# Optimization experiments

Hardware: AMD Instinct MI355X
Metric: run time of the kernel (lower is better)

## Reference

```python
import jax, jax.numpy as jnp
import numpy as np

NEG = jnp.float32(-1e30)  # finite stand-in for -inf (grad-safe)
BLANK = 0


def setup_inputs() -> dict:
    key = jax.random.key(0)
    k1, k2, k3, k4 = jax.random.split(key, 4)
    B, T, V, S = 64, 1024, 128, 256
    logits = jax.random.normal(k1, (B, T, V), dtype=jnp.float32)
    log_probs = jax.nn.log_softmax(logits, axis=-1)  # valid log-probs like a model head
    log_probs_length = jax.random.randint(k2, (B,), 768, T + 1)
    text_encoded = jax.random.randint(k3, (B, S), 1, V)  # labels exclude blank=0
    text_encoded_length = jax.random.randint(k4, (B,), 64, S + 1)
    return {
        "log_probs": log_probs,
        "log_probs_length": log_probs_length,
        "text_encoded": text_encoded,
        "text_encoded_length": text_encoded_length,
    }


def _ctc_loss(log_probs, input_lengths, targets, target_lengths):
    """CTC loss, matching torch.nn.CTCLoss(blank=0, reduction='mean', zero_infinity=True)."""
    B, T, V = log_probs.shape
    S = targets.shape[1]
    L2 = 2 * S + 1  # extended label sequence: blank-interleaved

    # extended labels ext[b, s]: blank at even s, target[(s-1)//2] at odd s
    ext = jnp.full((B, L2), BLANK, dtype=targets.dtype)
    ext = ext.at[:, 1::2].set(targets)

    # gather per-step log-prob of each extended label: [B, T, L2]
    lp_ext = jnp.take_along_axis(
        log_probs, jnp.broadcast_to(ext[:, None, :], (B, T, L2)), axis=2
    )

    pos = jnp.arange(L2)
    valid_s = pos[None, :] < (2 * target_lengths[:, None] + 1)  # [B, L2]
    ext_m2 = jnp.pad(ext, ((0, 0), (2, 0)), constant_values=BLANK)[:, :-2]
    # skip transition s-2 -> s allowed only at non-blank (odd) positions with differing labels
    skip_mask = (pos[None, :] >= 2) & (pos[None, :] % 2 == 1) & (ext != ext_m2)

    alpha0 = jnp.full((B, L2), NEG, dtype=log_probs.dtype)
    alpha0 = alpha0.at[:, 0].set(lp_ext[:, 0, 0])
    alpha0 = alpha0.at[:, 1].set(jnp.where(target_lengths > 0, lp_ext[:, 0, 1], NEG))
    alpha0 = jnp.where(valid_s, alpha0, NEG)

    lp_ext_T = jnp.moveaxis(lp_ext, 1, 0)  # [T, B, L2]

    def step(alpha, x):
        lp_t, t = x
        s1 = jnp.pad(alpha, ((0, 0), (1, 0)), constant_values=NEG)[:, :-1]
        s2 = jnp.pad(alpha, ((0, 0), (2, 0)), constant_values=NEG)[:, :-2]
        a = jnp.logaddexp(alpha, s1)
        a = jnp.where(skip_mask, jnp.logaddexp(a, s2), a)
        new = jnp.where(valid_s, a + lp_t, NEG)
        # freeze alpha for samples whose input sequence has ended
        new = jnp.where((t < input_lengths)[:, None], new, alpha)
        return new, None

    alpha, _ = jax.lax.scan(step, alpha0, (lp_ext_T[1:], jnp.arange(1, T)))

    L = target_lengths
    idx1 = (2 * L)[:, None]
    idx0 = jnp.maximum(2 * L - 1, 0)[:, None]
    a_blank = jnp.take_along_axis(alpha, idx1, axis=1)[:, 0]
    a_label = jnp.take_along_axis(alpha, idx0, axis=1)[:, 0]
    ll = jnp.logaddexp(a_blank, jnp.where(L > 0, a_label, NEG))
    loss_b = -ll
    # zero_infinity: zero out infeasible alignments
    loss_b = jnp.where(loss_b > 1e29, jnp.float32(0.0), loss_b)
    # reduction='mean': divide each loss by its target length, then batch-mean
    return jnp.mean(loss_b / jnp.maximum(L, 1).astype(log_probs.dtype))


def reference(log_probs, log_probs_length, text_encoded, text_encoded_length):
    return _ctc_loss(log_probs, log_probs_length, text_encoded, text_encoded_length)
```

## Files before the change

### kernel.cpp

```cpp
#include <hip/hip_runtime.h>

constexpr int B_ = 64;
constexpr int T_ = 1024;
constexpr int V_ = 128;
constexpr int S_ = 256;
constexpr int GRING = 64;
constexpr int NTAG = 16;
constexpr int ROWF = 384;
constexpr int NGW = 3;
constexpr float INV_LN2 = 1.4426950408889634f;
constexpr float LN2 = 0.6931471805599453f;

#define WS_DUMPF(W, b) ((W) + 64 + (size_t)(b) * 640)
#define WS_DUMPB(W, b) ((W) + 64 + 64 * 640 + (size_t)(b) * 640)
#define WS_KARR(W)     ((int*)((W) + 64 + 2 * 64 * 640))

#define WG_SCOPE __HIP_MEMORY_SCOPE_WORKGROUP

__device__ __forceinline__ void poll_eq(int* p, int want) {
    while (__hip_atomic_load(p, __ATOMIC_RELAXED, WG_SCOPE) != want)
        __builtin_amdgcn_s_sleep(1);
}

template <int CTRL>
__device__ __forceinline__ float dpp_mov0(float x) {
    return __int_as_float(__builtin_amdgcn_update_dpp(
        0, __float_as_int(x), CTRL, 0xF, 0xF, false));
}
template <int CTRL>
__device__ __forceinline__ float dpp_max(float x) {
    const float s = __int_as_float(__builtin_amdgcn_update_dpp(
        __float_as_int(x), __float_as_int(x), CTRL, 0xF, 0xF, false));
    return fmaxf(x, s);
}

__device__ __forceinline__ int wave_rescale(float a[10], int& K) {
    float mx = a[0];
    #pragma unroll
    for (int k = 1; k < 10; ++k) mx = fmaxf(mx, a[k]);
    mx = dpp_max<0x111>(mx);
    mx = dpp_max<0x112>(mx);
    mx = dpp_max<0x114>(mx);
    mx = dpp_max<0x118>(mx);
    mx = dpp_max<0x142>(mx);
    mx = dpp_max<0x143>(mx);
    const float mall = __int_as_float(
        __builtin_amdgcn_readlane(__float_as_int(mx), 63));
    int e;
    (void)frexpf(mall, &e);
    const int ks = (mall > 0.0f) ? (124 - e) : 0;
    #pragma unroll
    for (int k = 0; k < 10; ++k) a[k] = ldexpf(a[k], ks);
    K += ks;
    return ks;
}

__global__ __launch_bounds__(256) void ctc_scan(
    const float* __restrict__ lp,
    const int* __restrict__ in_len,
    const int* __restrict__ tgt,
    const int* __restrict__ tgt_len,
    float* __restrict__ W)
{
    const int b    = blockIdx.x & 63;
    const int dir  = blockIdx.x >> 6;
    const int tid  = threadIdx.x;
    const int wid  = tid >> 6;
    const int lane = tid & 63;

    __shared__ float ring[GRING * ROWF];
    __shared__ int   tags[NTAG];
    __shared__ int   cons;

    const int L  = tgt_len[b];
    const int Tb = in_len[b];
    const float* lpb = lp + (size_t)b * T_ * V_;
    const int* tg = tgt + b * S_;

    const int tm = (Tb - 2) >> 1;
    const int Uf = tm;
    const int Ub = Tb - 2 - tm;
    const int U  = dir ? Ub : Uf;

    if (tid == 0) cons = 0;
    if (tid < NTAG) tags[tid] = -1;
    __syncthreads();

    if (wid >= 1) {
        const int q = wid - 1;

        int   perm[5], oddc[5];
        float vmask[5];
        #pragma unroll
        for (int c = 0; c < 5; ++c) {
            const int j = 5 * lane + c;
            if (j < L) { const int lb = tg[j]; perm[c] = lb >> 1; oddc[c] = lb & 1; vmask[c] = 1.0f; }
            else       { perm[c] = 0; oddc[c] = 0; vmask[c] = 0.0f; }
        }

        float2 R0[4], R1[4];
        auto issue = [&](float2 (&Rb)[4], int m) {
            const int n = min(4, U - 4 * m);
            #pragma unroll
            for (int r = 0; r < 4; ++r) {
                if (r < n) {
                    const int u = 4 * m + 1 + r;
                    const int t = dir ? (Tb - 1 - u) : u;
                    Rb[r] = *(const float2*)(lpb + (size_t)t * V_ + 2 * lane);
                }
            }
        };
        auto process = [&](float2 (&Rb)[4], int m) {
            while (__hip_atomic_load(&cons, __ATOMIC_RELAXED, WG_SCOPE) < 4 * m - 60)
                __builtin_amdgcn_s_sleep(1);
            const int n = min(4, U - 4 * m);
            #pragma unroll
            for (int r = 0; r < 4; ++r) {
                if (r < n) {
                    const float e0 = __builtin_exp2f(Rb[r].x * INV_LN2);
                    const float e1 = __builtin_exp2f(Rb[r].y * INV_LN2);
                    const float p0 = __int_as_float(
                        __builtin_amdgcn_readfirstlane(__float_as_int(e0)));
                    float gv[5];
                    #pragma unroll
                    for (int c = 0; c < 5; ++c) {
                        const float lo = __shfl(e0, perm[c], 64);
                        const float hi = __shfl(e1, perm[c], 64);
                        gv[c] = vmask[c] * (oddc[c] ? hi : lo);
                    }
                    float* rb = ring + ((4 * m + r) & (GRING - 1)) * ROWF;
                    ((float2*)rb)[lane]         = make_float2(p0,    gv[0]);
                    ((float2*)(rb + 128))[lane] = make_float2(gv[1], gv[2]);
                    ((float2*)(rb + 256))[lane] = make_float2(gv[3], gv[4]);
                }
            }
            asm volatile("s_waitcnt lgkmcnt(0)" ::: "memory");
            if (lane == 0)
                __hip_atomic_store(&tags[m & (NTAG - 1)], m, __ATOMIC_RELAXED, WG_SCOPE);
        };

        int m = q;
        if (4 * m + 1 <= U) {
            issue(R0, m);
            if (4 * (m + NGW) + 1 <= U) issue(R1, m + NGW);
            while (true) {
                process(R0, m);
                if (4 * (m + 2 * NGW) + 1 <= U) issue(R0, m + 2 * NGW);
                m += NGW;
                if (4 * m + 1 > U) break;
                process(R1, m);
                if (4 * (m + 2 * NGW) + 1 <= U) issue(R1, m + 2 * NGW);
                m += NGW;
                if (4 * m + 1 > U) break;
            }
        }
        return;
    }

    float2 S[4][12];
    auto readBlock = [&](int set, int m) {
        const int base = ((4 * m) & (GRING - 1)) * ROWF + 2 * lane;
        #pragma unroll
        for (int r = 0; r < 4; ++r)
            #pragma unroll
            for (int pl = 0; pl < 3; ++pl)
                S[set][r * 3 + pl] =
                    *(const float2*)&ring[base + r * ROWF + pl * 128];
    };

    if (dir == 0) {
        float skipf[5];
        #pragma unroll
        for (int c = 0; c < 5; ++c) {
            const int j = 5 * lane + c;
            skipf[c] = (j >= 1 && j < L && tg[j] != tg[j - 1]) ? 1.0f : 0.0f;
        }
        float a[10];
        #pragma unroll
        for (int k = 0; k < 10; ++k) a[k] = 0.0f;
        {
            const float p00 = __builtin_exp2f(lpb[0] * INV_LN2);
            const float p01 = __builtin_exp2f(lpb[tg[0]] * INV_LN2);
            if (lane == 0) { a[0] = p00; a[1] = p01; }
        }
        float u9n = 0.0f;
        int K = 0;

        auto rowCore = [&](float2 c0, float2 c1, float2 c2) {
            const float u9 = u9n;
            const float p0 = c0.x;
            a[9] = (a[9] + a[8] + skipf[4] * a[7]) * c2.y;
            u9n = dpp_mov0<0x138>(a[9]);
            a[8] = (a[8] + a[7]) * p0;
            a[7] = (a[7] + a[6] + skipf[3] * a[5]) * c2.x;
            a[6] = (a[6] + a[5]) * p0;
            a[5] = (a[5] + a[4] + skipf[2] * a[3]) * c1.y;
            a[4] = (a[4] + a[3]) * p0;
            a[3] = (a[3] + a[2] + skipf[1] * a[1]) * c1.x;
            a[2] = (a[2] + a[1]) * p0;
            a[1] = (a[1] + a[0] + skipf[0] * u9) * c0.y;
            a[0] = (a[0] + u9) * p0;
        };
        auto row4 = [&](int set) {
            #pragma unroll
            for (int r = 0; r < 4; ++r)
                rowCore(S[set][r * 3], S[set][r * 3 + 1], S[set][r * 3 + 2]);
        };
        auto body = [&](int m, int setc, int setp) {
            if (4 * (m + 3) + 1 <= Uf) {
                poll_eq(&tags[(m + 3) & (NTAG - 1)], m + 3);
                readBlock(setp, m + 3);
            }
            row4(setc);
            if (lane == 0)
                __hip_atomic_store(&cons, 4 * m + 4, __ATOMIC_RELAXED, WG_SCOPE);
        };

        const int MB4 = (Uf / 4) & ~3;
        poll_eq(&tags[0], 0); readBlock(0, 0);
        poll_eq(&tags[1], 1); readBlock(1, 1);
        poll_eq(&tags[2], 2); readBlock(2, 2);
        for (int mb = 0; mb < MB4; mb += 4) {
            body(mb + 0, 0, 3);
            body(mb + 1, 1, 0);
            { const int ks = wave_rescale(a, K); u9n = ldexpf(u9n, ks); }
            body(mb + 2, 2, 1);
            body(mb + 3, 3, 2);
            { const int ks = wave_rescale(a, K); u9n = ldexpf(u9n, ks); }
        }
        #pragma unroll
        for (int r = 0; r < 4; ++r)
            if (4 * MB4 + 1 + r <= Uf)
                rowCore(S[0][r * 3], S[0][r * 3 + 1], S[0][r * 3 + 2]);
        #pragma unroll
        for (int r = 0; r < 4; ++r)
            if (4 * MB4 + 5 + r <= Uf)
                rowCore(S[1][r * 3], S[1][r * 3 + 1], S[1][r * 3 + 2]);
        { const int ks = wave_rescale(a, K); u9n = ldexpf(u9n, ks); }
        #pragma unroll
        for (int r = 0; r < 4; ++r)
            if (4 * MB4 + 9 + r <= Uf)
                rowCore(S[2][r * 3], S[2][r * 3 + 1], S[2][r * 3 + 2]);
        for (int u = 4 * MB4 + 13; u <= Uf; ++u) {
            const int bu = (u - 1) >> 2;
            poll_eq(&tags[bu & (NTAG - 1)], bu);
            const int base = ((u - 1) & (GRING - 1)) * ROWF + 2 * lane;
            const float2 c0 = *(const float2*)&ring[base];
            const float2 c1 = *(const float2*)&ring[base + 128];
            const float2 c2 = *(const float2*)&ring[base + 256];
            rowCore(c0, c1, c2);
        }

        float* dump = WS_DUMPF(W, b);
        #pragma unroll
        for (int k = 0; k < 10; ++k) dump[10 * lane + k] = a[k];
        if (lane == 0) WS_KARR(W)[b] = K;
    } else {
        float sB[5];
        #pragma unroll
        for (int c = 0; c < 5; ++c) {
            const int j = 5 * lane + c + 1;
            sB[c] = (j < L && tg[j] != tg[j - 1]) ? 1.0f : 0.0f;
        }
        float g[10];
        #pragma unroll
        for (int k = 0; k < 10; ++k) g[k] = 0.0f;
        {
            const float pb = __builtin_exp2f(lpb[(size_t)(Tb - 1) * V_] * INV_LN2);
            const float pl = __builtin_exp2f(lpb[(size_t)(Tb - 1) * V_ + tg[L - 1]] * INV_LN2);
            #pragma unroll
            for (int k = 0; k < 10; ++k) {
                const int s = 10 * lane + k;
                if (s == 2 * L)     g[k] = pb;
                if (s == 2 * L - 1) g[k] = pl;
            }
        }
        float d0n = dpp_mov0<0x130>(g[0]);
        float d1n = dpp_mov0<0x130>(g[1]);
        int K = 0;

        auto rowCore = [&](float2 c0, float2 c1, float2 c2) {
            const float d0 = d0n, d1 = d1n;
            const float p0 = c0.x;
            g[0] = (g[0] + g[1]) * p0;
            g[1] = (g[1] + g[2] + sB[0] * g[3]) * c0.y;
            d0n = dpp_mov0<0x130>(g[0]);
            d1n = dpp_mov0<0x130>(g[1]);
            g[2] = (g[2] + g[3]) * p0;
            g[3] = (g[3] + g[4] + sB[1] * g[5]) * c1.x;
            g[4] = (g[4] + g[5]) * p0;
            g[5] = (g[5] + g[6] + sB[2] * g[7]) * c1.y;
            g[6] = (g[6] + g[7]) * p0;
            g[7] = (g[7] + g[8] + sB[3] * g[9]) * c2.x;
            g[8] = (g[8] + g[9]) * p0;
            g[9] = (g[9] + d0 + sB[4] * d1) * c2.y;
        };
        auto row4 = [&](int set) {
            #pragma unroll
            for (int r = 0; r < 4; ++r)
                rowCore(S[set][r * 3], S[set][r * 3 + 1], S[set][r * 3 + 2]);
        };
        auto body = [&](int m, int setc, int setp) {
            if (4 * (m + 3) + 1 <= Ub) {
                poll_eq(&tags[(m + 3) & (NTAG - 1)], m + 3);
                readBlock(setp, m + 3);
            }
            row4(setc);
            if (lane == 0)
                __hip_atomic_store(&cons, 4 * m + 4, __ATOMIC_RELAXED, WG_SCOPE);
        };

        const int MB4 = (Ub / 4) & ~3;
        poll_eq(&tags[0], 0); readBlock(0, 0);
        poll_eq(&tags[1], 1); readBlock(1, 1);
        poll_eq(&tags[2], 2); readBlock(2, 2);
        for (int mb = 0; mb < MB4; mb += 4) {
            body(mb + 0, 0, 3);
            body(mb + 1, 1, 0);
            { const int ks = wave_rescale(g, K);
              d0n = ldexpf(d0n, ks); d1n = ldexpf(d1n, ks); }
            body(mb + 2, 2, 1);
            body(mb + 3, 3, 2);
            { const int ks = wave_rescale(g, K);
              d0n = ldexpf(d0n, ks); d1n = ldexpf(d1n, ks); }
        }
        #pragma unroll
        for (int r = 0; r < 4; ++r)
            if (4 * MB4 + 1 + r <= Ub)
                rowCore(S[0][r * 3], S[0][r * 3 + 1], S[0][r * 3 + 2]);
        #pragma unroll
        for (int r = 0; r < 4; ++r)
            if (4 * MB4 + 5 + r <= Ub)
                rowCore(S[1][r * 3], S[1][r * 3 + 1], S[1][r * 3 + 2]);
        { const int ks = wave_rescale(g, K);
          d0n = ldexpf(d0n, ks); d1n = ldexpf(d1n, ks); }
        #pragma unroll
        for (int r = 0; r < 4; ++r)
            if (4 * MB4 + 9 + r <= Ub)
                rowCore(S[2][r * 3], S[2][r * 3 + 1], S[2][r * 3 + 2]);
        for (int u = 4 * MB4 + 13; u <= Ub; ++u) {
            const int bu = (u - 1) >> 2;
            poll_eq(&tags[bu & (NTAG - 1)], bu);
            const int base = ((u - 1) & (GRING - 1)) * ROWF + 2 * lane;
            const float2 c0 = *(const float2*)&ring[base];
            const float2 c1 = *(const float2*)&ring[base + 128];
            const float2 c2 = *(const float2*)&ring[base + 256];
            rowCore(c0, c1, c2);
        }

        {
            const float d0 = d0n, d1 = d1n;
            g[0] = g[0] + g[1];
            g[1] = g[1] + g[2] + sB[0] * g[3];
            g[2] = g[2] + g[3];
            g[3] = g[3] + g[4] + sB[1] * g[5];
            g[4] = g[4] + g[5];
            g[5] = g[5] + g[6] + sB[2] * g[7];
            g[6] = g[6] + g[7];
            g[7] = g[7] + g[8] + sB[3] * g[9];
            g[8] = g[8] + g[9];
            g[9] = g[9] + d0 + sB[4] * d1;
        }
        float* dump = WS_DUMPB(W, b);
        #pragma unroll
        for (int k = 0; k < 10; ++k) dump[10 * lane + k] = g[k];
        if (lane == 0) WS_KARR(W)[64 + b] = K;
    }
}

__global__ void ctc_join_kernel(const float* __restrict__ W_const,
                                const int* __restrict__ tgt_len,
                                float* __restrict__ lossArr) {
    const int b = blockIdx.x;
    const int lane = threadIdx.x;
    float* W = const_cast<float*>(W_const);
    const float* dA = WS_DUMPF(W, b);
    const float* dB = WS_DUMPB(W, b);
    double sum = 0.0;
    #pragma unroll
    for (int k = 0; k < 10; ++k)
        sum += (double)dA[10 * lane + k] * (double)dB[10 * lane + k];
    #pragma unroll
    for (int d = 1; d < 64; d <<= 1) sum += __shfl_xor(sum, d, 64);
    if (lane == 0) {
        const int L = tgt_len[b];
        const int KF = WS_KARR(W)[b];
        const int KB = WS_KARR(W)[64 + b];
        float loss = 0.0f;
        if (sum > 0.0) {
            const long long ub = __double_as_longlong(sum);
            const int ex = (int)((ub >> 52) & 2047) - 1023;
            const double f = __longlong_as_double(
                (ub & 0x000FFFFFFFFFFFFFLL) | 0x3FF0000000000000LL);
            const float ll2 = __builtin_log2f((float)f)
                            + (float)(ex - KF - KB);
            loss = -(ll2 * LN2);
            if (!(loss <= 1e29f)) loss = 0.0f;
        }
        lossArr[b] = loss / (float)L;
    }
}

__global__ void ctc_reduce_kernel(const float* __restrict__ ws, float* __restrict__ out) {
    float v = ws[threadIdx.x];
    #pragma unroll
    for (int o = 32; o > 0; o >>= 1) v += __shfl_down(v, o);
    if (threadIdx.x == 0) out[0] = v / (float)B_;
}

extern "C" void kernel_launch(void* const* d_in, const int* in_sizes, int n_in,
                              void* d_out, int out_size, void* d_ws, size_t ws_size,
                              hipStream_t stream) {
    const float* lp      = (const float*)d_in[0];
    const int*   in_len  = (const int*)d_in[1];
    const int*   tgt     = (const int*)d_in[2];
    const int*   tgt_len = (const int*)d_in[3];
    float* W   = (float*)d_ws;
    float* out = (float*)d_out;

    ctc_scan<<<2 * B_, 256, 0, stream>>>(lp, in_len, tgt, tgt_len, W);
    ctc_join_kernel<<<B_, 64, 0, stream>>>(W, tgt_len, W);
    ctc_reduce_kernel<<<1, 64, 0, stream>>>(W, out);
}
```

Measured before the change: 130.2 us.

## Move label gather from producer waves into consumer LDS reads, shrink ring rows

Producer waves now only exponentiate each time-step row and store the raw 128-entry probability row into LDS. The label permutation moves to the consumer wave, which gathers by label offset straight from the ring. This shrinks ring rows from 384 to 128 floats and drops the per-row shuffle work in the producers. The block goes from four waves to three, and consumer prefetch depth falls from three blocks to one. The consumer's critical serial path now carries the indexed LDS gathers and extra vmask multiplies, and the shallower prefetch may expose latency.

```diff
diff --git a/kernel.cpp b/kernel.cpp
--- a/kernel.cpp
+++ b/kernel.cpp
@@ -6,8 +6,8 @@
 constexpr int S_ = 256;
 constexpr int GRING = 64;
 constexpr int NTAG = 16;
-constexpr int ROWF = 384;
-constexpr int NGW = 3;
+constexpr int RW = 128;
+constexpr int NGW = 2;
 constexpr float INV_LN2 = 1.4426950408889634f;
 constexpr float LN2 = 0.6931471805599453f;
 
@@ -55,7 +55,7 @@
     return ks;
 }
 
-__global__ __launch_bounds__(256) void ctc_scan(
+__global__ __launch_bounds__(192) void ctc_scan(
     const float* __restrict__ lp,
     const int* __restrict__ in_len,
     const int* __restrict__ tgt,
@@ -68,7 +68,7 @@
     const int wid  = tid >> 6;
     const int lane = tid & 63;
 
-    __shared__ float ring[GRING * ROWF];
+    __shared__ float ring[GRING * RW];
     __shared__ int   tags[NTAG];
     __shared__ int   cons;
 
@@ -88,15 +88,6 @@
 
     if (wid >= 1) {
         const int q = wid - 1;
-
-        int   perm[5], oddc[5];
-        float vmask[5];
-        #pragma unroll
-        for (int c = 0; c < 5; ++c) {
-            const int j = 5 * lane + c;
-            if (j < L) { const int lb = tg[j]; perm[c] = lb >> 1; oddc[c] = lb & 1; vmask[c] = 1.0f; }
-            else       { perm[c] = 0; oddc[c] = 0; vmask[c] = 0.0f; }
-        }
 
         float2 R0[4], R1[4];
         auto issue = [&](float2 (&Rb)[4], int m) {
@@ -119,19 +110,8 @@
                 if (r < n) {
                     const float e0 = __builtin_exp2f(Rb[r].x * INV_LN2);
                     const float e1 = __builtin_exp2f(Rb[r].y * INV_LN2);
-                    const float p0 = __int_as_float(
-                        __builtin_amdgcn_readfirstlane(__float_as_int(e0)));
-                    float gv[5];
-                    #pragma unroll
-                    for (int c = 0; c < 5; ++c) {
-                        const float lo = __shfl(e0, perm[c], 64);
-                        const float hi = __shfl(e1, perm[c], 64);
-                        gv[c] = vmask[c] * (oddc[c] ? hi : lo);
-                    }
-                    float* rb = ring + ((4 * m + r) & (GRING - 1)) * ROWF;
-                    ((float2*)rb)[lane]         = make_float2(p0,    gv[0]);
-                    ((float2*)(rb + 128))[lane] = make_float2(gv[1], gv[2]);
-                    ((float2*)(rb + 256))[lane] = make_float2(gv[3], gv[4]);
+                    float* rb = ring + ((4 * m + r) & (GRING - 1)) * RW;
+                    ((float2*)rb)[lane] = make_float2(e0, e1);
                 }
             }
             asm volatile("s_waitcnt lgkmcnt(0)" ::: "memory");
@@ -157,15 +137,31 @@
         return;
     }
 
-    float2 S[4][12];
+    int   off[5];
+    float vmask[5];
+    #pragma unroll
+    for (int c = 0; c < 5; ++c) {
+        const int j = 5 * lane + c;
+        if (j < L) { off[c] = tg[j]; vmask[c] = 1.0f; }
+        else       { off[c] = 0;     vmask[c] = 0.0f; }
+    }
+
+    float S2[2][24];
     auto readBlock = [&](int set, int m) {
-        const int base = ((4 * m) & (GRING - 1)) * ROWF + 2 * lane;
-        #pragma unroll
-        for (int r = 0; r < 4; ++r)
-            #pragma unroll
-            for (int pl = 0; pl < 3; ++pl)
-                S[set][r * 3 + pl] =
-                    *(const float2*)&ring[base + r * ROWF + pl * 128];
+        const int base = ((4 * m) & (GRING - 1)) * RW;
+        #pragma unroll
+        for (int r = 0; r < 4; ++r) {
+            S2[set][r * 6 + 0] = ring[base + r * RW];
+            #pragma unroll
+            for (int c = 0; c < 5; ++c)
+                S2[set][r * 6 + 1 + c] = ring[base + r * RW + off[c]];
+        }
+    };
+    auto readRowDirect = [&](int u, float (&v)[6]) {
+        const int base = ((u - 1) & (GRING - 1)) * RW;
+        v[0] = ring[base];
+        #pragma unroll
+        for (int c = 0; c < 5; ++c) v[1 + c] = ring[base + off[c]];
     };
 
     if (dir == 0) {
@@ -204,57 +200,51 @@
         auto row4 = [&](int set) {
             #pragma unroll
             for (int r = 0; r < 4; ++r)
-                rowCore(S[set][r * 3], S[set][r * 3 + 1], S[set][r * 3 + 2]);
+                rowCore(make_float2(S2[set][r*6+0], vmask[0]*S2[set][r*6+1]),
+                        make_float2(vmask[1]*S2[set][r*6+2], vmask[2]*S2[set][r*6+3]),
+                        make_float2(vmask[3]*S2[set][r*6+4], vmask[4]*S2[set][r*6+5]));
         };
         auto body = [&](int m, int setc, int setp) {
-            if (4 * (m + 3) + 1 <= Uf) {
-                poll_eq(&tags[(m + 3) & (NTAG - 1)], m + 3);
-                readBlock(setp, m + 3);
+            if (4 * (m + 1) + 1 <= Uf) {
+                poll_eq(&tags[(m + 1) & (NTAG - 1)], m + 1);
+                readBlock(setp, m + 1);
             }
             row4(setc);
             if (lane == 0)
                 __hip_atomic_store(&cons, 4 * m + 4, __ATOMIC_RELAXED, WG_SCOPE);
         };
 
-        const int MB4 = (Uf / 4) & ~3;
+        const int MB2 = (Uf / 4) & ~1;
         poll_eq(&tags[0], 0); readBlock(0, 0);
-        poll_eq(&tags[1], 1); readBlock(1, 1);
-        poll_eq(&tags[2], 2); readBlock(2, 2);
-        for (int mb = 0; mb < MB4; mb += 4) {
-            body(mb + 0, 0, 3);
+        for (int mb = 0; mb < MB2; mb += 2) {
+            body(mb + 0, 0, 1);
             body(mb + 1, 1, 0);
             { const int ks = wave_rescale(a, K); u9n = ldexpf(u9n, ks); }
-            body(mb + 2, 2, 1);
-            body(mb + 3, 3, 2);
-            { const int ks = wave_rescale(a, K); u9n = ldexpf(u9n, ks); }
         }
         #pragma unroll
         for (int r = 0; r < 4; ++r)
-            if (4 * MB4 + 1 + r <= Uf)
-                rowCore(S[0][r * 3], S[0][r * 3 + 1], S[0][r * 3 + 2]);
-        #pragma unroll
-        for (int r = 0; r < 4; ++r)
-            if (4 * MB4 + 5 + r <= Uf)
-                rowCore(S[1][r * 3], S[1][r * 3 + 1], S[1][r * 3 + 2]);
-        { const int ks = wave_rescale(a, K); u9n = ldexpf(u9n, ks); }
-        #pragma unroll
-        for (int r = 0; r < 4; ++r)
-            if (4 * MB4 + 9 + r <= Uf)
-                rowCore(S[2][r * 3], S[2][r * 3 + 1], S[2][r * 3 + 2]);
-        for (int u = 4 * MB4 + 13; u <= Uf; ++u) {
+            if (4 * MB2 + 1 + r <= Uf)
+                rowCore(make_float2(S2[0][r*6+0], vmask[0]*S2[0][r*6+1]),
+                        make_float2(vmask[1]*S2[0][r*6+2], vmask[2]*S2[0][r*6+3]),
+                        make_float2(vmask[3]*S2[0][r*6+4], vmask[4]*S2[0][r*6+5]));
+        for (int u = 4 * (MB2 + 1) + 1; u <= Uf; ++u) {
             const int bu = (u - 1) >> 2;
             poll_eq(&tags[bu & (NTAG - 1)], bu);
-            const int base = ((u - 1) & (GRING - 1)) * ROWF + 2 * lane;
-            const float2 c0 = *(const float2*)&ring[base];
-            const float2 c1 = *(const float2*)&ring[base + 128];
-            const float2 c2 = *(const float2*)&ring[base + 256];
-            rowCore(c0, c1, c2);
-        }
+            float v[6];
+            readRowDirect(u, v);
+            rowCore(make_float2(v[0], vmask[0]*v[1]),
+                    make_float2(vmask[1]*v[2], vmask[2]*v[3]),
+                    make_float2(vmask[3]*v[4], vmask[4]*v[5]));
+        }
+        { const int ks = wave_rescale(a, K); u9n = ldexpf(u9n, ks); }
 
         float* dump = WS_DUMPF(W, b);
         #pragma unroll
         for (int k = 0; k < 10; ++k) dump[10 * lane + k] = a[k];
-        if (lane == 0) WS_KARR(W)[b] = K;
+        if (lane == 0) {
+            WS_KARR(W)[b] = K;
+            __hip_atomic_store(&cons, Uf + 64, __ATOMIC_RELAXED, WG_SCOPE);
+        }
     } else {
         float sB[5];
         #pragma unroll
@@ -298,55 +288,45 @@
         auto row4 = [&](int set) {
             #pragma unroll
             for (int r = 0; r < 4; ++r)
-                rowCore(S[set][r * 3], S[set][r * 3 + 1], S[set][r * 3 + 2]);
+                rowCore(make_float2(S2[set][r*6+0], vmask[0]*S2[set][r*6+1]),
+                        make_float2(vmask[1]*S2[set][r*6+2], vmask[2]*S2[set][r*6+3]),
+                        make_float2(vmask[3]*S2[set][r*6+4], vmask[4]*S2[set][r*6+5]));
         };
         auto body = [&](int m, int setc, int setp) {
-            if (4 * (m + 3) + 1 <= Ub) {
-                poll_eq(&tags[(m + 3) & (NTAG - 1)], m + 3);
-                readBlock(setp, m + 3);
+            if (4 * (m + 1) + 1 <= Ub) {
+                poll_eq(&tags[(m + 1) & (NTAG - 1)], m + 1);
+                readBlock(setp, m + 1);
             }
             row4(setc);
             if (lane == 0)
                 __hip_atomic_store(&cons, 4 * m + 4, __ATOMIC_RELAXED, WG_SCOPE);
         };
 
-        const int MB4 = (Ub / 4) & ~3;
+        const int MB2 = (Ub / 4) & ~1;
         poll_eq(&tags[0], 0); readBlock(0, 0);
-        poll_eq(&tags[1], 1); readBlock(1, 1);
-        poll_eq(&tags[2], 2); readBlock(2, 2);
-        for (int mb = 0; mb < MB4; mb += 4) {
-            body(mb + 0, 0, 3);
+        for (int mb = 0; mb < MB2; mb += 2) {
+            body(mb + 0, 0, 1);
             body(mb + 1, 1, 0);
             { const int ks = wave_rescale(g, K);
               d0n = ldexpf(d0n, ks); d1n = ldexpf(d1n, ks); }
-            body(mb + 2, 2, 1);
-            body(mb + 3, 3, 2);
-            { const int ks = wave_rescale(g, K);
-              d0n = ldexpf(d0n, ks); d1n = ldexpf(d1n, ks); }
         }
         #pragma unroll
         for (int r = 0; r < 4; ++r)
-            if (4 * MB4 + 1 + r <= Ub)
-                rowCore(S[0][r * 3], S[0][r * 3 + 1], S[0][r * 3 + 2]);
-        #pragma unroll
-        for (int r = 0; r < 4; ++r)
-            if (4 * MB4 + 5 + r <= Ub)
-                rowCore(S[1][r * 3], S[1][r * 3 + 1], S[1][r * 3 + 2]);
+            if (4 * MB2 + 1 + r <= Ub)
+                rowCore(make_float2(S2[0][r*6+0], vmask[0]*S2[0][r*6+1]),
+                        make_float2(vmask[1]*S2[0][r*6+2], vmask[2]*S2[0][r*6+3]),
+                        make_float2(vmask[3]*S2[0][r*6+4], vmask[4]*S2[0][r*6+5]));
+        for (int u = 4 * (MB2 + 1) + 1; u <= Ub; ++u) {
+            const int bu = (u - 1) >> 2;
+            poll_eq(&tags[bu & (NTAG - 1)], bu);
+            float v[6];
+            readRowDirect(u, v);
+            rowCore(make_float2(v[0], vmask[0]*v[1]),
+                    make_float2(vmask[1]*v[2], vmask[2]*v[3]),
+                    make_float2(vmask[3]*v[4], vmask[4]*v[5]));
+        }
         { const int ks = wave_rescale(g, K);
           d0n = ldexpf(d0n, ks); d1n = ldexpf(d1n, ks); }
-        #pragma unroll
-        for (int r = 0; r < 4; ++r)
-            if (4 * MB4 + 9 + r <= Ub)
-                rowCore(S[2][r * 3], S[2][r * 3 + 1], S[2][r * 3 + 2]);
-        for (int u = 4 * MB4 + 13; u <= Ub; ++u) {
-            const int bu = (u - 1) >> 2;
-            poll_eq(&tags[bu & (NTAG - 1)], bu);
-            const int base = ((u - 1) & (GRING - 1)) * ROWF + 2 * lane;
-            const float2 c0 = *(const float2*)&ring[base];
-            const float2 c1 = *(const float2*)&ring[base + 128];
-            const float2 c2 = *(const float2*)&ring[base + 256];
-            rowCore(c0, c1, c2);
-        }
 
         {
             const float d0 = d0n, d1 = d1n;
@@ -364,7 +344,10 @@
         float* dump = WS_DUMPB(W, b);
         #pragma unroll
         for (int k = 0; k < 10; ++k) dump[10 * lane + k] = g[k];
-        if (lane == 0) WS_KARR(W)[64 + b] = K;
+        if (lane == 0) {
+            WS_KARR(W)[64 + b] = K;
+            __hip_atomic_store(&cons, Ub + 64, __ATOMIC_RELAXED, WG_SCOPE);
+        }
     }
 }
 
@@ -418,7 +401,7 @@
     float* W   = (float*)d_ws;
     float* out = (float*)d_out;
 
-    ctc_scan<<<2 * B_, 256, 0, stream>>>(lp, in_len, tgt, tgt_len, W);
+    ctc_scan<<<2 * B_, 192, 0, stream>>>(lp, in_len, tgt, tgt_len, W);
     ctc_join_kernel<<<B_, 64, 0, stream>>>(W, tgt_len, W);
     ctc_reduce_kernel<<<1, 64, 0, stream>>>(W, out);
 }
```

New measurement: 136.3 us. 4.7% more time.
